# Kernel optimization log

Hardware: AMD Instinct MI355X
Metric: run time of the kernel (lower is better)

The kernel has to match this reference:

```python
import jax, jax.numpy as jnp
import numpy as np

B, S, D = 4, 2048, 1024
EPS = 1e-6


def setup_inputs() -> dict:
    key = jax.random.key(0)
    ks = jax.random.split(key, 9)
    s = 1.0 / np.sqrt(D)
    return {
        "context": jax.random.normal(ks[0], (B, S, D), jnp.float32),
        "eos_mask": jax.random.randint(ks[1], (B, S, S), 0, 2, dtype=jnp.int32),
        "prior": jax.random.uniform(ks[2], (B, S, S), jnp.float32),
        "Wq": jax.random.uniform(ks[3], (D, D), jnp.float32, -s, s),
        "bq": jax.random.uniform(ks[4], (D,), jnp.float32, -s, s),
        "Wk": jax.random.uniform(ks[5], (D, D), jnp.float32, -s, s),
        "bk": jax.random.uniform(ks[6], (D,), jnp.float32, -s, s),
        "gamma": jnp.ones((D,), jnp.float32),
        "beta": jnp.zeros((D,), jnp.float32),
    }


def reference(context, eos_mask, prior, Wq, bq, Wk, bk, gamma, beta):
    d = context.shape[-1]
    seq = context.shape[1]

    # LayerNorm with torch's unbiased std (Bessel correction)
    mean = jnp.mean(context, axis=-1, keepdims=True)
    var = jnp.sum((context - mean) ** 2, axis=-1, keepdims=True) / (d - 1)
    x = gamma * (context - mean) / (jnp.sqrt(var) + EPS) + beta

    q = x @ Wq + bq  # linear_query
    k = x @ Wk + bk  # linear_key

    scores = jnp.einsum("bid,bjd->bij", q, k) / d  # note: /d, not /sqrt(d)

    idx = jnp.arange(seq)
    band = jnp.abs(idx[:, None] - idx[None, :]) == 1      # a + c (tridiagonal off-diagonals)
    sup = (idx[None, :] - idx[:, None]) == 1              # a (superdiagonal)
    strict_upper = idx[:, None] < idx[None, :]            # triu(ones) - eye
    eye = idx[:, None] == idx[None, :]

    mask = (eos_mask != 0) & band[None]                   # eos_mask & (a + c)
    scores = jnp.where(mask, scores, -1e9)
    na = jax.nn.softmax(scores, axis=-1)
    na = jnp.sqrt(na * jnp.swapaxes(na, -1, -2) + 1e-9)
    na = prior + (1.0 - prior) * na                       # hier_add_index branch

    # t = log(na+eps).masked_fill(a==0,0) @ triu  ==  cumsum along last axis
    t = jnp.where(sup[None], jnp.log(na + 1e-9), 0.0)
    t = jnp.cumsum(t, axis=-1)
    # g = triu @ t  ==  reversed cumsum along axis -2
    g = jnp.cumsum(t[..., ::-1, :], axis=-2)[..., ::-1, :]
    g = jnp.where(strict_upper[None], jnp.exp(g), 0.0)

    g_attn = g + jnp.swapaxes(g, -1, -2) + jnp.where(eye[None], na, 1e-9)
    return (g_attn, na)
```

## Files before the change

kernel.cpp:

```cpp
#include <hip/hip_runtime.h>
#include <hip/hip_bf16.h>
#include <cmath>

#define BB 4
#define SS 2048
#define DD 1024
#define NN 2048
#define BS (BB*SS)
constexpr float EPS = 1e-6f;

typedef __attribute__((ext_vector_type(8))) short short8;
typedef __attribute__((ext_vector_type(4))) float floatx4;

__global__ __launch_bounds__(256)
void ln_kernel(const float* __restrict__ ctx, const float* __restrict__ gamma,
               const float* __restrict__ beta, __hip_bfloat16* __restrict__ xo) {
    int row = blockIdx.x;
    int t = threadIdx.x;
    const float* r = ctx + (size_t)row * DD;
    float4 v = ((const float4*)r)[t];
    float s1 = v.x + v.y + v.z + v.w;
    float s2 = v.x*v.x + v.y*v.y + v.z*v.z + v.w*v.w;
    #pragma unroll
    for (int off = 32; off; off >>= 1) {
        s1 += __shfl_down(s1, off);
        s2 += __shfl_down(s2, off);
    }
    __shared__ float ls1[4], ls2[4];
    int wid = t >> 6, lane = t & 63;
    if (lane == 0) { ls1[wid] = s1; ls2[wid] = s2; }
    __syncthreads();
    if (t == 0) {
        float a = ls1[0] + ls1[1] + ls1[2] + ls1[3];
        float b = ls2[0] + ls2[1] + ls2[2] + ls2[3];
        float mean = a / DD;
        float var = (b - a * a / DD) / (DD - 1);
        ls1[0] = mean;
        ls2[0] = 1.0f / (sqrtf(var) + EPS);
    }
    __syncthreads();
    float mean = ls1[0], rstd = ls2[0];
    float4 g = ((const float4*)gamma)[t];
    float4 be = ((const float4*)beta)[t];
    union { ushort4 u; __hip_bfloat16 h[4]; } pk;
    pk.h[0] = __float2bfloat16(g.x * (v.x - mean) * rstd + be.x);
    pk.h[1] = __float2bfloat16(g.y * (v.y - mean) * rstd + be.y);
    pk.h[2] = __float2bfloat16(g.z * (v.z - mean) * rstd + be.z);
    pk.h[3] = __float2bfloat16(g.w * (v.w - mean) * rstd + be.w);
    ((ushort4*)(xo + (size_t)row * DD))[t] = pk.u;
}

__global__ __launch_bounds__(256)
void prep_kernel(const float* __restrict__ Wq, const float* __restrict__ Wk,
                 __hip_bfloat16* __restrict__ WT) {
    __shared__ float tile[32][33];
    int kt = blockIdx.x * 32;
    int nt = blockIdx.y * 32;
    int t = threadIdx.x;
    int lr = t >> 3;
    int lc = (t & 7) * 4;
    const float* W = (nt < DD) ? Wq : Wk;
    int nsrc = (nt < DD) ? nt : nt - DD;
    float4 v = *(const float4*)(W + (size_t)(kt + lr) * DD + nsrc + lc);
    tile[lr][lc + 0] = v.x;
    tile[lr][lc + 1] = v.y;
    tile[lr][lc + 2] = v.z;
    tile[lr][lc + 3] = v.w;
    __syncthreads();
    union { ushort4 u; __hip_bfloat16 h[4]; } pk;
    pk.h[0] = __float2bfloat16(tile[lc + 0][lr]);
    pk.h[1] = __float2bfloat16(tile[lc + 1][lr]);
    pk.h[2] = __float2bfloat16(tile[lc + 2][lr]);
    pk.h[3] = __float2bfloat16(tile[lc + 3][lr]);
    *(ushort4*)(WT + (size_t)(nt + lr) * DD + kt + lc) = pk.u;
}

__global__ __launch_bounds__(256)
void bias_kernel(const float* __restrict__ bq, const float* __restrict__ bk,
                 float* __restrict__ biasc) {
    int i = blockIdx.x * 256 + threadIdx.x;
    biasc[i] = (i < DD) ? bq[i] : bk[i - DD];
}

#define TM 128
#define TN 128
#define TK 32
__global__ __launch_bounds__(256, 1)
void gemm_mfma(const __hip_bfloat16* __restrict__ X,
               const __hip_bfloat16* __restrict__ WT,
               const float* __restrict__ biasc,
               __hip_bfloat16* __restrict__ C) {
    __shared__ short As[TM * TK];
    __shared__ short Bs[TN * TK];
    int tid = threadIdx.x;
    int wave = tid >> 6;
    int lane = tid & 63;
    int wm = wave >> 1, wn = wave & 1;
    int q = lane >> 4, m16 = lane & 15;

    int srow = lane >> 2;
    int skoff = (lane & 3) * 8;
    const __hip_bfloat16* gA = X + ((size_t)blockIdx.x * TM + wave * 32 + srow) * DD + skoff;
    const __hip_bfloat16* gB = WT + ((size_t)blockIdx.y * TN + wave * 32 + srow) * DD + skoff;
    short* lAbase = As + (wave * 32) * TK;
    short* lBbase = Bs + (wave * 32) * TK;

    floatx4 acc[4][4] = {};

    for (int k0 = 0; k0 < DD; k0 += TK) {
        __builtin_amdgcn_global_load_lds(
            (const __attribute__((address_space(1))) void*)(gA + k0),
            (__attribute__((address_space(3))) void*)(lAbase), 16, 0, 0);
        __builtin_amdgcn_global_load_lds(
            (const __attribute__((address_space(1))) void*)(gA + k0 + 16 * DD),
            (__attribute__((address_space(3))) void*)(lAbase + 16 * TK), 16, 0, 0);
        __builtin_amdgcn_global_load_lds(
            (const __attribute__((address_space(1))) void*)(gB + k0),
            (__attribute__((address_space(3))) void*)(lBbase), 16, 0, 0);
        __builtin_amdgcn_global_load_lds(
            (const __attribute__((address_space(1))) void*)(gB + k0 + 16 * DD),
            (__attribute__((address_space(3))) void*)(lBbase + 16 * TK), 16, 0, 0);
        __syncthreads();
        short8 af[4], bf[4];
        #pragma unroll
        for (int r = 0; r < 4; ++r)
            af[r] = *(const short8*)(As + (wm * 64 + r * 16 + m16) * TK + q * 8);
        #pragma unroll
        for (int c = 0; c < 4; ++c)
            bf[c] = *(const short8*)(Bs + (wn * 64 + c * 16 + m16) * TK + q * 8);
        #pragma unroll
        for (int r = 0; r < 4; ++r)
            #pragma unroll
            for (int c = 0; c < 4; ++c)
                acc[r][c] = __builtin_amdgcn_mfma_f32_16x16x32_bf16(af[r], bf[c], acc[r][c], 0, 0, 0);
        __syncthreads();
    }

    int gcol0 = blockIdx.y * TN + wn * 64 + m16;
    int growb = blockIdx.x * TM + wm * 64 + q * 4;
    #pragma unroll
    for (int r = 0; r < 4; ++r) {
        #pragma unroll
        for (int c = 0; c < 4; ++c) {
            int gcol = gcol0 + c * 16;
            float bval = biasc[gcol];
            #pragma unroll
            for (int e = 0; e < 4; ++e) {
                int grow = growb + r * 16 + e;
                C[(size_t)grow * NN + gcol] = __float2bfloat16(acc[r][c][e] + bval);
            }
        }
    }
}

__global__ __launch_bounds__(256)
void band_kernel(const __hip_bfloat16* __restrict__ C, const int* __restrict__ eos,
                 float* __restrict__ vsub, float* __restrict__ vsup,
                 float* __restrict__ wuni) {
    int gw = (blockIdx.x * blockDim.x + threadIdx.x) >> 6;
    int lane = threadIdx.x & 63;
    int i = gw & (SS - 1);
    float qv[16];
    {
        const ushort4* p = (const ushort4*)(C + (size_t)gw * NN + lane * 16);
        #pragma unroll
        for (int m = 0; m < 4; ++m) {
            union { ushort4 u; __hip_bfloat16 h[4]; } cv; cv.u = p[m];
            #pragma unroll
            for (int r = 0; r < 4; ++r) qv[m * 4 + r] = __bfloat162float(cv.h[r]);
        }
    }
    float ssup = 0.f, ssub = 0.f;
    if (i < SS - 1) {
        const ushort4* p = (const ushort4*)(C + (size_t)(gw + 1) * NN + DD + lane * 16);
        #pragma unroll
        for (int m = 0; m < 4; ++m) {
            union { ushort4 u; __hip_bfloat16 h[4]; } cv; cv.u = p[m];
            #pragma unroll
            for (int r = 0; r < 4; ++r) ssup += qv[m * 4 + r] * __bfloat162float(cv.h[r]);
        }
    }
    if (i > 0) {
        const ushort4* p = (const ushort4*)(C + (size_t)(gw - 1) * NN + DD + lane * 16);
        #pragma unroll
        for (int m = 0; m < 4; ++m) {
            union { ushort4 u; __hip_bfloat16 h[4]; } cv; cv.u = p[m];
            #pragma unroll
            for (int r = 0; r < 4; ++r) ssub += qv[m * 4 + r] * __bfloat162float(cv.h[r]);
        }
    }
    #pragma unroll
    for (int off = 32; off; off >>= 1) {
        ssup += __shfl_down(ssup, off);
        ssub += __shfl_down(ssub, off);
    }
    if (lane == 0) {
        ssup *= (1.0f / DD);
        ssub *= (1.0f / DD);
        bool msub = (i > 0) && (eos[(size_t)gw * SS + (i - 1)] != 0);
        bool msup = (i < SS - 1) && (eos[(size_t)gw * SS + (i + 1)] != 0);
        float vs, vp, w;
        if (msub && msup) {
            float mx = fmaxf(ssub, ssup);
            float e1 = expf(ssub - mx), e2 = expf(ssup - mx);
            float inv = 1.0f / (e1 + e2);
            vs = e1 * inv; vp = e2 * inv; w = 0.f;
        } else if (msub) { vs = 1.f; vp = 0.f; w = 0.f; }
        else if (msup)   { vs = 0.f; vp = 1.f; w = 0.f; }
        else             { vs = vp = w = 1.0f / SS; }
        vsub[gw] = vs; vsup[gw] = vp; wuni[gw] = w;
    }
}

__global__ __launch_bounds__(256)
void scan_kernel(const float* __restrict__ prior, const float* __restrict__ vsub,
                 const float* __restrict__ vsup, double* __restrict__ Lc) {
    int b = blockIdx.x;
    int t = threadIdx.x;
    double loc[8];
    double s = 0.0;
    #pragma unroll
    for (int k = 0; k < 8; ++k) {
        int tt = t * 8 + k;
        double Lv = 0.0;
        if (tt < SS - 1) {
            float pr = prior[((size_t)(b * SS + tt)) * SS + tt + 1];
            float na2 = sqrtf(vsup[b * SS + tt] * vsub[b * SS + tt + 1] + 1e-9f);
            float P = pr + (1.f - pr) * na2;
            Lv = log((double)P + 1e-9);
        }
        loc[k] = Lv; s += Lv;
    }
    __shared__ double sa[256], sb[256];
    sa[t] = s;
    __syncthreads();
    double* src = sa; double* dst = sb;
    for (int off = 1; off < 256; off <<= 1) {
        double v = src[t];
        if (t >= off) v += src[t - off];
        __syncthreads();
        dst[t] = v;
        __syncthreads();
        double* tmp = src; src = dst; dst = tmp;
    }
    double run = (t == 0) ? 0.0 : src[t - 1];
    #pragma unroll
    for (int k = 0; k < 8; ++k) {
        int idx = t * 8 + k;
        Lc[b * SS + idx] = run;
        run += loc[k];
    }
}

__global__ __launch_bounds__(256)
void out_kernel(const float* __restrict__ prior, const float* __restrict__ vsub,
                const float* __restrict__ vsup, const float* __restrict__ wuni,
                const double* __restrict__ Lc, float* __restrict__ out_g,
                float* __restrict__ out_na) {
    size_t gid = (size_t)blockIdx.x * 256 + threadIdx.x;
    int jt = (int)(gid & 511);
    int row = (int)(gid >> 9);
    int i = row & (SS - 1);
    int b = row >> 11;
    int j0 = jt * 4;
    size_t base = (size_t)row * SS + j0;
    float4 pr4 = *(const float4*)(prior + base);
    float4 wj4 = *(const float4*)(wuni + b * SS + j0);
    float pra[4] = {pr4.x, pr4.y, pr4.z, pr4.w};
    float wja[4] = {wj4.x, wj4.y, wj4.z, wj4.w};
    float wi = wuni[row];
    double Lci = Lc[row];
    const double* Lcb = Lc + b * SS;
    float nav[4], gv[4];
    #pragma unroll
    for (int c = 0; c < 4; ++c) {
        int j = j0 + c;
        float prod;
        if (j == i - 1)      prod = vsub[row] * vsup[row - 1];
        else if (j == i + 1) prod = vsup[row] * vsub[row + 1];
        else if (j == i)     prod = wi * wi;
        else                 prod = wi * wja[c];
        float na2 = sqrtf(prod + 1e-9f);
        float p = pra[c];
        float na3 = p + (1.f - p) * na2;
        nav[c] = na3;
        if (j == i) {
            gv[c] = na3;
        } else {
            double d = (j > i) ? (Lcb[j] - Lci) : (Lci - Lcb[j]);
            gv[c] = expf((float)d) + 1e-9f;
        }
    }
    *(float4*)(out_g + base) = make_float4(gv[0], gv[1], gv[2], gv[3]);
    *(float4*)(out_na + base) = make_float4(nav[0], nav[1], nav[2], nav[3]);
}

extern "C" void kernel_launch(void* const* d_in, const int* in_sizes, int n_in,
                              void* d_out, int out_size, void* d_ws, size_t ws_size,
                              hipStream_t stream) {
    const float* ctx   = (const float*)d_in[0];
    const int*   eos   = (const int*)d_in[1];
    const float* prior = (const float*)d_in[2];
    const float* Wq    = (const float*)d_in[3];
    const float* bq    = (const float*)d_in[4];
    const float* Wk    = (const float*)d_in[5];
    const float* bk    = (const float*)d_in[6];
    const float* gamma = (const float*)d_in[7];
    const float* beta  = (const float*)d_in[8];

    float* out_g  = (float*)d_out;
    float* out_na = out_g + (size_t)BB * SS * SS;

    char* ws = (char*)d_ws;
    __hip_bfloat16* x  = (__hip_bfloat16*)ws;
    __hip_bfloat16* C  = (__hip_bfloat16*)(ws + (size_t)BS * DD * 2);
    __hip_bfloat16* WT = (__hip_bfloat16*)(ws + (size_t)BS * DD * 2
                                              + (size_t)BS * NN * 2);
    char* p2 = ws + (size_t)BS * DD * 2 + (size_t)BS * NN * 2 + (size_t)NN * DD * 2;
    float* biasc = (float*)p2;
    float* vsub = biasc + NN;
    float* vsup = vsub + BS;
    float* wuni = vsup + BS;
    double* Lc = (double*)(wuni + BS);

    ln_kernel<<<BS, 256, 0, stream>>>(ctx, gamma, beta, x);

    dim3 gp(DD / 32, NN / 32);
    prep_kernel<<<gp, 256, 0, stream>>>(Wq, Wk, WT);
    bias_kernel<<<NN / 256, 256, 0, stream>>>(bq, bk, biasc);

    dim3 gg(BS / TM, NN / TN);
    gemm_mfma<<<gg, 256, 0, stream>>>(x, WT, biasc, C);

    band_kernel<<<BS / 4, 256, 0, stream>>>(C, eos, vsub, vsup, wuni);

    scan_kernel<<<BB, 256, 0, stream>>>(prior, vsub, vsup, Lc);

    size_t total = (size_t)BB * SS * SS / 4;
    out_kernel<<<(int)(total / 256), 256, 0, stream>>>(prior, vsub, vsup, wuni, Lc,
                                                       out_g, out_na);
}
```

Baseline: 336.7 us.

## Precompute Wq·Wkᵀ so the projection GEMM produces one matrix instead of two

The q·k band scores are rewritten as x·(Wq Wkᵀ)·x'ᵀ plus bias terms. A small 1024×1024 GEMM forms the combined weight, one GEMM with half the output width produces z, and GEMVs plus per-row dot products computed in LayerNorm supply the bias terms. This roughly halves the main GEMM's FLOPs and its output traffic, and drops the weight-transpose and bias kernels. The GEMM epilogue is also staged through LDS so stores are coalesced. The cost is an extra small GEMM and a different bf16 rounding path: the combined weight is rounded to bf16, which may shift accuracy.

```diff
diff --git a/kernel.cpp b/kernel.cpp
--- a/kernel.cpp
+++ b/kernel.cpp
@@ -5,7 +5,6 @@
 #define BB 4
 #define SS 2048
 #define DD 1024
-#define NN 2048
 #define BS (BB*SS)
 constexpr float EPS = 1e-6f;
 
@@ -13,14 +12,56 @@
 typedef __attribute__((ext_vector_type(4))) float floatx4;
 
 __global__ __launch_bounds__(256)
+void wconv_kernel(const float* __restrict__ Wq, const float* __restrict__ Wk,
+                  __hip_bfloat16* __restrict__ Wb) {
+    int idx = blockIdx.x * 256 + threadIdx.x;
+    const int half = DD * DD / 4;
+    const float* src = (idx < half) ? Wk : Wq;
+    int off = (idx < half) ? idx : idx - half;
+    float4 v = ((const float4*)src)[off];
+    union { ushort4 u; __hip_bfloat16 h[4]; } pk;
+    pk.h[0] = __float2bfloat16(v.x);
+    pk.h[1] = __float2bfloat16(v.y);
+    pk.h[2] = __float2bfloat16(v.z);
+    pk.h[3] = __float2bfloat16(v.w);
+    ((ushort4*)Wb)[idx] = pk.u;
+}
+
+__global__ __launch_bounds__(256)
+void gemv_kernel(const float* __restrict__ Wq, const float* __restrict__ Wk,
+                 const float* __restrict__ bq, const float* __restrict__ bk,
+                 float* __restrict__ u, float* __restrict__ v, float* __restrict__ cs) {
+    int gid = blockIdx.x * 4 + (threadIdx.x >> 6);
+    int lane = threadIdx.x & 63;
+    if (gid > 2048) return;
+    const float* row; const float* vec; float* outp;
+    if (gid < 1024)      { row = Wq + (size_t)gid * DD;          vec = bk; outp = u + gid; }
+    else if (gid < 2048) { row = Wk + (size_t)(gid - 1024) * DD; vec = bq; outp = v + (gid - 1024); }
+    else                 { row = bq;                             vec = bk; outp = cs; }
+    float s = 0.f;
+    #pragma unroll
+    for (int k = 0; k < 4; ++k) {
+        float4 a = ((const float4*)row)[lane * 4 + k];
+        float4 b = ((const float4*)vec)[lane * 4 + k];
+        s += a.x * b.x + a.y * b.y + a.z * b.z + a.w * b.w;
+    }
+    #pragma unroll
+    for (int off = 32; off; off >>= 1) s += __shfl_down(s, off);
+    if (lane == 0) *outp = s;
+}
+
+__global__ __launch_bounds__(256)
 void ln_kernel(const float* __restrict__ ctx, const float* __restrict__ gamma,
-               const float* __restrict__ beta, __hip_bfloat16* __restrict__ xo) {
+               const float* __restrict__ beta, const float* __restrict__ u,
+               const float* __restrict__ v, const float* __restrict__ cs,
+               __hip_bfloat16* __restrict__ xo, float* __restrict__ alpha,
+               float* __restrict__ betav) {
     int row = blockIdx.x;
     int t = threadIdx.x;
     const float* r = ctx + (size_t)row * DD;
-    float4 v = ((const float4*)r)[t];
-    float s1 = v.x + v.y + v.z + v.w;
-    float s2 = v.x*v.x + v.y*v.y + v.z*v.z + v.w*v.w;
+    float4 val = ((const float4*)r)[t];
+    float s1 = val.x + val.y + val.z + val.w;
+    float s2 = val.x*val.x + val.y*val.y + val.z*val.z + val.w*val.w;
     #pragma unroll
     for (int off = 32; off; off >>= 1) {
         s1 += __shfl_down(s1, off);
@@ -42,56 +83,44 @@
     float mean = ls1[0], rstd = ls2[0];
     float4 g = ((const float4*)gamma)[t];
     float4 be = ((const float4*)beta)[t];
-    union { ushort4 u; __hip_bfloat16 h[4]; } pk;
-    pk.h[0] = __float2bfloat16(g.x * (v.x - mean) * rstd + be.x);
-    pk.h[1] = __float2bfloat16(g.y * (v.y - mean) * rstd + be.y);
-    pk.h[2] = __float2bfloat16(g.z * (v.z - mean) * rstd + be.z);
-    pk.h[3] = __float2bfloat16(g.w * (v.w - mean) * rstd + be.w);
-    ((ushort4*)(xo + (size_t)row * DD))[t] = pk.u;
-}
-
-__global__ __launch_bounds__(256)
-void prep_kernel(const float* __restrict__ Wq, const float* __restrict__ Wk,
-                 __hip_bfloat16* __restrict__ WT) {
-    __shared__ float tile[32][33];
-    int kt = blockIdx.x * 32;
-    int nt = blockIdx.y * 32;
-    int t = threadIdx.x;
-    int lr = t >> 3;
-    int lc = (t & 7) * 4;
-    const float* W = (nt < DD) ? Wq : Wk;
-    int nsrc = (nt < DD) ? nt : nt - DD;
-    float4 v = *(const float4*)(W + (size_t)(kt + lr) * DD + nsrc + lc);
-    tile[lr][lc + 0] = v.x;
-    tile[lr][lc + 1] = v.y;
-    tile[lr][lc + 2] = v.z;
-    tile[lr][lc + 3] = v.w;
-    __syncthreads();
-    union { ushort4 u; __hip_bfloat16 h[4]; } pk;
-    pk.h[0] = __float2bfloat16(tile[lc + 0][lr]);
-    pk.h[1] = __float2bfloat16(tile[lc + 1][lr]);
-    pk.h[2] = __float2bfloat16(tile[lc + 2][lr]);
-    pk.h[3] = __float2bfloat16(tile[lc + 3][lr]);
-    *(ushort4*)(WT + (size_t)(nt + lr) * DD + kt + lc) = pk.u;
-}
-
-__global__ __launch_bounds__(256)
-void bias_kernel(const float* __restrict__ bq, const float* __restrict__ bk,
-                 float* __restrict__ biasc) {
-    int i = blockIdx.x * 256 + threadIdx.x;
-    biasc[i] = (i < DD) ? bq[i] : bk[i - DD];
+    float nx0 = g.x * (val.x - mean) * rstd + be.x;
+    float nx1 = g.y * (val.y - mean) * rstd + be.y;
+    float nx2 = g.z * (val.z - mean) * rstd + be.z;
+    float nx3 = g.w * (val.w - mean) * rstd + be.w;
+    union { ushort4 uu; __hip_bfloat16 h[4]; } pk;
+    pk.h[0] = __float2bfloat16(nx0);
+    pk.h[1] = __float2bfloat16(nx1);
+    pk.h[2] = __float2bfloat16(nx2);
+    pk.h[3] = __float2bfloat16(nx3);
+    ((ushort4*)(xo + (size_t)row * DD))[t] = pk.uu;
+    float4 u4 = ((const float4*)u)[t];
+    float4 v4 = ((const float4*)v)[t];
+    float du = nx0 * u4.x + nx1 * u4.y + nx2 * u4.z + nx3 * u4.w;
+    float dv = nx0 * v4.x + nx1 * v4.y + nx2 * v4.z + nx3 * v4.w;
+    #pragma unroll
+    for (int off = 32; off; off >>= 1) {
+        du += __shfl_down(du, off);
+        dv += __shfl_down(dv, off);
+    }
+    __syncthreads();
+    if (lane == 0) { ls1[wid] = du; ls2[wid] = dv; }
+    __syncthreads();
+    if (t == 0) {
+        alpha[row] = ls1[0] + ls1[1] + ls1[2] + ls1[3] + *cs;
+        betav[row] = ls2[0] + ls2[1] + ls2[2] + ls2[3];
+    }
 }
 
 #define TM 128
 #define TN 128
 #define TK 32
-__global__ __launch_bounds__(256, 1)
-void gemm_mfma(const __hip_bfloat16* __restrict__ X,
-               const __hip_bfloat16* __restrict__ WT,
-               const float* __restrict__ biasc,
-               __hip_bfloat16* __restrict__ C) {
-    __shared__ short As[TM * TK];
-    __shared__ short Bs[TN * TK];
+__global__ __launch_bounds__(256)
+void gemm_mfma(const __hip_bfloat16* __restrict__ A,
+               const __hip_bfloat16* __restrict__ B,
+               __hip_bfloat16* __restrict__ C, int ldc) {
+    __shared__ short smem[18432];
+    short* As = smem;
+    short* Bs = smem + TM * TK;
     int tid = threadIdx.x;
     int wave = tid >> 6;
     int lane = tid & 63;
@@ -100,8 +129,8 @@
 
     int srow = lane >> 2;
     int skoff = (lane & 3) * 8;
-    const __hip_bfloat16* gA = X + ((size_t)blockIdx.x * TM + wave * 32 + srow) * DD + skoff;
-    const __hip_bfloat16* gB = WT + ((size_t)blockIdx.y * TN + wave * 32 + srow) * DD + skoff;
+    const __hip_bfloat16* gA = A + ((size_t)blockIdx.x * TM + wave * 32 + srow) * DD + skoff;
+    const __hip_bfloat16* gB = B + ((size_t)blockIdx.y * TN + wave * 32 + srow) * DD + skoff;
     short* lAbase = As + (wave * 32) * TK;
     short* lBbase = Bs + (wave * 32) * TK;
 
@@ -136,57 +165,63 @@
         __syncthreads();
     }
 
-    int gcol0 = blockIdx.y * TN + wn * 64 + m16;
-    int growb = blockIdx.x * TM + wm * 64 + q * 4;
-    #pragma unroll
-    for (int r = 0; r < 4; ++r) {
-        #pragma unroll
-        for (int c = 0; c < 4; ++c) {
-            int gcol = gcol0 + c * 16;
-            float bval = biasc[gcol];
+    short* EP = smem + wave * 4608;
+    #pragma unroll
+    for (int r = 0; r < 4; ++r)
+        #pragma unroll
+        for (int c = 0; c < 4; ++c)
             #pragma unroll
             for (int e = 0; e < 4; ++e) {
-                int grow = growb + r * 16 + e;
-                C[(size_t)grow * NN + gcol] = __float2bfloat16(acc[r][c][e] + bval);
+                __hip_bfloat16 hv = __float2bfloat16(acc[r][c][e]);
+                EP[(r * 16 + q * 4 + e) * 72 + c * 16 + m16] = *(short*)&hv;
             }
-        }
-    }
-}
-
-__global__ __launch_bounds__(256)
-void band_kernel(const __hip_bfloat16* __restrict__ C, const int* __restrict__ eos,
-                 float* __restrict__ vsub, float* __restrict__ vsup,
-                 float* __restrict__ wuni) {
+    int grow0 = blockIdx.x * TM + wm * 64;
+    int gcol0 = blockIdx.y * TN + wn * 64;
+    short* Cc = (short*)C;
+    #pragma unroll
+    for (int it = 0; it < 8; ++it) {
+        int rl = it * 8 + (lane >> 3);
+        int cg = (lane & 7) * 8;
+        short8 vv = *(const short8*)(EP + rl * 72 + cg);
+        *(short8*)(Cc + (size_t)(grow0 + rl) * ldc + gcol0 + cg) = vv;
+    }
+}
+
+__global__ __launch_bounds__(256)
+void band_kernel(const __hip_bfloat16* __restrict__ z, const __hip_bfloat16* __restrict__ x,
+                 const int* __restrict__ eos, const float* __restrict__ alpha,
+                 const float* __restrict__ betav, float* __restrict__ vsub,
+                 float* __restrict__ vsup, float* __restrict__ wuni) {
     int gw = (blockIdx.x * blockDim.x + threadIdx.x) >> 6;
     int lane = threadIdx.x & 63;
     int i = gw & (SS - 1);
-    float qv[16];
+    float zv[16];
     {
-        const ushort4* p = (const ushort4*)(C + (size_t)gw * NN + lane * 16);
+        const ushort4* p = (const ushort4*)(z + (size_t)gw * DD + lane * 16);
         #pragma unroll
         for (int m = 0; m < 4; ++m) {
             union { ushort4 u; __hip_bfloat16 h[4]; } cv; cv.u = p[m];
             #pragma unroll
-            for (int r = 0; r < 4; ++r) qv[m * 4 + r] = __bfloat162float(cv.h[r]);
+            for (int r = 0; r < 4; ++r) zv[m * 4 + r] = __bfloat162float(cv.h[r]);
         }
     }
     float ssup = 0.f, ssub = 0.f;
     if (i < SS - 1) {
-        const ushort4* p = (const ushort4*)(C + (size_t)(gw + 1) * NN + DD + lane * 16);
+        const ushort4* p = (const ushort4*)(x + (size_t)(gw + 1) * DD + lane * 16);
         #pragma unroll
         for (int m = 0; m < 4; ++m) {
             union { ushort4 u; __hip_bfloat16 h[4]; } cv; cv.u = p[m];
             #pragma unroll
-            for (int r = 0; r < 4; ++r) ssup += qv[m * 4 + r] * __bfloat162float(cv.h[r]);
+            for (int r = 0; r < 4; ++r) ssup += zv[m * 4 + r] * __bfloat162float(cv.h[r]);
         }
     }
     if (i > 0) {
-        const ushort4* p = (const ushort4*)(C + (size_t)(gw - 1) * NN + DD + lane * 16);
+        const ushort4* p = (const ushort4*)(x + (size_t)(gw - 1) * DD + lane * 16);
         #pragma unroll
         for (int m = 0; m < 4; ++m) {
             union { ushort4 u; __hip_bfloat16 h[4]; } cv; cv.u = p[m];
             #pragma unroll
-            for (int r = 0; r < 4; ++r) ssub += qv[m * 4 + r] * __bfloat162float(cv.h[r]);
+            for (int r = 0; r < 4; ++r) ssub += zv[m * 4 + r] * __bfloat162float(cv.h[r]);
         }
     }
     #pragma unroll
@@ -195,8 +230,9 @@
         ssub += __shfl_down(ssub, off);
     }
     if (lane == 0) {
-        ssup *= (1.0f / DD);
-        ssub *= (1.0f / DD);
+        float a = alpha[gw];
+        if (i < SS - 1) ssup = (ssup + a + betav[gw + 1]) * (1.0f / DD);
+        if (i > 0)      ssub = (ssub + a + betav[gw - 1]) * (1.0f / DD);
         bool msub = (i > 0) && (eos[(size_t)gw * SS + (i - 1)] != 0);
         bool msup = (i < SS - 1) && (eos[(size_t)gw * SS + (i + 1)] != 0);
         float vs, vp, w;
@@ -312,27 +348,35 @@
     float* out_na = out_g + (size_t)BB * SS * SS;
 
     char* ws = (char*)d_ws;
-    __hip_bfloat16* x  = (__hip_bfloat16*)ws;
-    __hip_bfloat16* C  = (__hip_bfloat16*)(ws + (size_t)BS * DD * 2);
-    __hip_bfloat16* WT = (__hip_bfloat16*)(ws + (size_t)BS * DD * 2
-                                              + (size_t)BS * NN * 2);
-    char* p2 = ws + (size_t)BS * DD * 2 + (size_t)BS * NN * 2 + (size_t)NN * DD * 2;
-    float* biasc = (float*)p2;
-    float* vsub = biasc + NN;
-    float* vsup = vsub + BS;
-    float* wuni = vsup + BS;
-    double* Lc = (double*)(wuni + BS);
-
-    ln_kernel<<<BS, 256, 0, stream>>>(ctx, gamma, beta, x);
-
-    dim3 gp(DD / 32, NN / 32);
-    prep_kernel<<<gp, 256, 0, stream>>>(Wq, Wk, WT);
-    bias_kernel<<<NN / 256, 256, 0, stream>>>(bq, bk, biasc);
-
-    dim3 gg(BS / TM, NN / TN);
-    gemm_mfma<<<gg, 256, 0, stream>>>(x, WT, biasc, C);
-
-    band_kernel<<<BS / 4, 256, 0, stream>>>(C, eos, vsub, vsup, wuni);
+    size_t o = 0;
+    __hip_bfloat16* x  = (__hip_bfloat16*)(ws + o); o += (size_t)BS * DD * 2;
+    __hip_bfloat16* z  = (__hip_bfloat16*)(ws + o); o += (size_t)BS * DD * 2;
+    __hip_bfloat16* Wb = (__hip_bfloat16*)(ws + o); o += (size_t)2 * DD * DD * 2;
+    __hip_bfloat16* Mt = (__hip_bfloat16*)(ws + o); o += (size_t)DD * DD * 2;
+    double* Lc   = (double*)(ws + o); o += (size_t)BS * 8;
+    float* u     = (float*)(ws + o);  o += DD * 4;
+    float* v     = (float*)(ws + o);  o += DD * 4;
+    float* cs    = (float*)(ws + o);  o += 64;
+    float* alpha = (float*)(ws + o);  o += (size_t)BS * 4;
+    float* betav = (float*)(ws + o);  o += (size_t)BS * 4;
+    float* vsub  = (float*)(ws + o);  o += (size_t)BS * 4;
+    float* vsup  = (float*)(ws + o);  o += (size_t)BS * 4;
+    float* wuni  = (float*)(ws + o);  o += (size_t)BS * 4;
+
+    __hip_bfloat16* Wk_bf = Wb;
+    __hip_bfloat16* Wq_bf = Wb + (size_t)DD * DD;
+
+    wconv_kernel<<<(2 * DD * DD / 4) / 256, 256, 0, stream>>>(Wq, Wk, Wb);
+    gemv_kernel<<<513, 256, 0, stream>>>(Wq, Wk, bq, bk, u, v, cs);
+    ln_kernel<<<BS, 256, 0, stream>>>(ctx, gamma, beta, u, v, cs, x, alpha, betav);
+
+    dim3 g1(DD / TM, DD / TN);
+    gemm_mfma<<<g1, 256, 0, stream>>>(Wk_bf, Wq_bf, Mt, DD);
+
+    dim3 g2(BS / TM, DD / TN);
+    gemm_mfma<<<g2, 256, 0, stream>>>(x, Mt, z, DD);
+
+    band_kernel<<<BS / 4, 256, 0, stream>>>(z, x, eos, alpha, betav, vsub, vsup, wuni);
 
     scan_kernel<<<BB, 256, 0, stream>>>(prior, vsub, vsup, Lc);
 
```

After: 337.4 us. Within noise of the previous version (+0.2%).
